# Optimization experiments

Hardware: AMD Instinct MI355X
Metric: run time of the kernel (lower is better)

## Reference

```python
import jax, jax.numpy as jnp
import numpy as np
import math

B, S, D, H = 2, 2048, 1024, 16
DK = D // H


def setup_inputs() -> dict:
    key = jax.random.key(0)
    ks = jax.random.split(key, 10)
    sc = 1.0 / math.sqrt(D)
    inp = {
        "Q_input": jax.random.normal(ks[0], (B, S, D), dtype=jnp.float32),
        "Wq_w": jax.random.normal(ks[1], (D, D), dtype=jnp.float32) * sc,
        "Wq_b": jnp.zeros((D,), dtype=jnp.float32),
        "Wk_w": jax.random.normal(ks[2], (D, D), dtype=jnp.float32) * sc,
        "Wk_b": jnp.zeros((D,), dtype=jnp.float32),
        "Wv_w": jax.random.normal(ks[3], (D, D), dtype=jnp.float32) * sc,
        "Wv_b": jnp.zeros((D,), dtype=jnp.float32),
        "Wo_w": jax.random.normal(ks[4], (D, D), dtype=jnp.float32) * sc,
        "Wo_b": jnp.zeros((D,), dtype=jnp.float32),
        # causal mask, broadcast over batch and heads: [1,1,S,S]
        "mask": jnp.tril(jnp.ones((S, S), dtype=jnp.int32))[None, None],
    }
    return inp


def reference(Q_input, Wq_w, Wq_b, Wk_w, Wk_b, Wv_w, Wv_b, Wo_w, Wo_b, mask):
    b, s, _ = Q_input.shape
    # linear projections (torch Linear: x @ W^T + b)
    Q = Q_input @ Wq_w.T + Wq_b
    K = Q_input @ Wk_w.T + Wk_b
    V = Q_input @ Wv_w.T + Wv_b
    # [b, h, s, dk]
    Q = Q.reshape(b, s, H, DK).transpose(0, 2, 1, 3)
    K = K.reshape(b, s, H, DK).transpose(0, 2, 1, 3)
    V = V.reshape(b, s, H, DK).transpose(0, 2, 1, 3)
    scores = jnp.einsum("bhqd,bhkd->bhqk", Q, K) / math.sqrt(DK)
    scores = jnp.where(mask == 0, jnp.float32(-1e9), scores)
    weights = jax.nn.softmax(scores, axis=-1)
    attn = jnp.einsum("bhqk,bhkd->bhqd", weights, V)
    attn = attn.transpose(0, 2, 1, 3).reshape(b, s, D)
    return attn @ Wo_w.T + Wo_b
```

## Files before the change

### kernel.cpp

```cpp
#include <hip/hip_runtime.h>
#include <hip/hip_bf16.h>
#include <cstdint>

typedef __attribute__((ext_vector_type(8))) short short8;
typedef __attribute__((ext_vector_type(4))) float f32x4;
typedef __attribute__((ext_vector_type(2))) unsigned int uint2v;
typedef unsigned short ushort_t;

#define S_LEN 2048
#define D_DIM 1024
#define NH 16
#define DK 64
#define BATCH 2
#define M_ROWS (BATCH * S_LEN)
#define BK 32

__device__ inline ushort_t f2bf(float f) {
    union { float f; uint32_t u; } v; v.f = f;
    uint32_t r = v.u + 0x7fffu + ((v.u >> 16) & 1u);
    return (ushort_t)(r >> 16);
}

__device__ __forceinline__ ushort_t bfc(float f) {
    __hip_bfloat16 h = __float2bfloat16(f);
    return __builtin_bit_cast(ushort_t, h);
}

__device__ __forceinline__ void glds16(const ushort_t* g, ushort_t* l) {
    __builtin_amdgcn_global_load_lds(
        (const __attribute__((address_space(1))) uint32_t*)g,
        (__attribute__((address_space(3))) uint32_t*)l,
        16, 0, 0);
}

__device__ __forceinline__ float red_max4(float x) {
#if __has_builtin(__builtin_amdgcn_permlane16_swap) && __has_builtin(__builtin_amdgcn_permlane32_swap)
    uint2v a = __builtin_amdgcn_permlane16_swap(__float_as_uint(x), __float_as_uint(x), false, false);
    float y = fmaxf(__uint_as_float(a.x), __uint_as_float(a.y));
    uint2v b = __builtin_amdgcn_permlane32_swap(__float_as_uint(y), __float_as_uint(y), false, false);
    return fmaxf(__uint_as_float(b.x), __uint_as_float(b.y));
#else
    x = fmaxf(x, __shfl_xor(x, 16));
    return fmaxf(x, __shfl_xor(x, 32));
#endif
}
__device__ __forceinline__ float red_sum4(float x) {
#if __has_builtin(__builtin_amdgcn_permlane16_swap) && __has_builtin(__builtin_amdgcn_permlane32_swap)
    uint2v a = __builtin_amdgcn_permlane16_swap(__float_as_uint(x), __float_as_uint(x), false, false);
    float y = __uint_as_float(a.x) + __uint_as_float(a.y);
    uint2v b = __builtin_amdgcn_permlane32_swap(__float_as_uint(y), __float_as_uint(y), false, false);
    return __uint_as_float(b.x) + __uint_as_float(b.y);
#else
    x += __shfl_xor(x, 16);
    return x + __shfl_xor(x, 32);
#endif
}

__global__ void cvt_bf16(const float* __restrict__ in, ushort_t* __restrict__ out, int n4) {
    int i = blockIdx.x * blockDim.x + threadIdx.x;
    int stride = gridDim.x * blockDim.x;
    for (int idx = i; idx < n4; idx += stride) {
        float4 v = ((const float4*)in)[idx];
        ushort4 o;
        o.x = f2bf(v.x); o.y = f2bf(v.y); o.z = f2bf(v.z); o.w = f2bf(v.w);
        ((ushort4*)out)[idx] = o;
    }
}

__global__ void cvt_w3(const float* __restrict__ wq, const float* __restrict__ wk,
                       const float* __restrict__ wv, ushort_t* __restrict__ wqkv) {
    const int seg = (D_DIM * D_DIM) / 4;
    int i = blockIdx.x * blockDim.x + threadIdx.x;
    int stride = gridDim.x * blockDim.x;
    for (int idx = i; idx < 3 * seg; idx += stride) {
        int sel = idx >> 18;
        int id = idx & (seg - 1);
        const float* src = sel == 0 ? wq : (sel == 1 ? wk : wv);
        float4 v = ((const float4*)src)[id];
        ushort4 o;
        o.x = f2bf(v.x); o.y = f2bf(v.y); o.z = f2bf(v.z); o.w = f2bf(v.w);
        ((ushort4*)wqkv)[sel * seg + id] = o;
    }
}

template<int MODE, int BMt, int BNt>
__global__ __launch_bounds__(256) void gemm_bt(const ushort_t* __restrict__ A,
                                               const ushort_t* __restrict__ Bw,
                                               const float* __restrict__ b0,
                                               const float* __restrict__ b1,
                                               const float* __restrict__ b2,
                                               void* __restrict__ C0,
                                               void* __restrict__ C1,
                                               void* __restrict__ C2,
                                               int M, int N, int K) {
    constexpr int FM = BMt / 32, FN = BNt / 32;
    constexpr int ACH = BMt / 64, BCH = BNt / 64;
    __shared__ ushort_t As[BMt * BK];
    __shared__ ushort_t Bs[BNt * BK];
    int tid = threadIdx.x;
    int lane = tid & 63;
    int w = tid >> 6;
    int wr = w >> 1, wc = w & 1;
    int ntile = N / BNt;
    int m0 = (blockIdx.x / ntile) * BMt;
    int n0 = (blockIdx.x % ntile) * BNt;
    int lr = lane & 15;
    int lk = (lane >> 4) * 8;
    int srow = lane >> 2;
    int scol = (lane & 3) * 8;

    f32x4 acc[FM][FN] = {};

    for (int kt = 0; kt < K; kt += BK) {
        __syncthreads();
#pragma unroll
        for (int c = 0; c < ACH; c++)
            glds16(&A[(size_t)(m0 + w * (BMt / 4) + c * 16 + srow) * K + kt + scol],
                   &As[(w * (BMt / 4) + c * 16) * BK]);
#pragma unroll
        for (int c = 0; c < BCH; c++)
            glds16(&Bw[(size_t)(n0 + w * (BNt / 4) + c * 16 + srow) * K + kt + scol],
                   &Bs[(w * (BNt / 4) + c * 16) * BK]);
        __syncthreads();

        short8 af[FM], bf[FN];
#pragma unroll
        for (int f = 0; f < FM; f++)
            af[f] = *(const short8*)&As[(wr * (BMt / 2) + f * 16 + lr) * BK + lk];
#pragma unroll
        for (int f = 0; f < FN; f++)
            bf[f] = *(const short8*)&Bs[(wc * (BNt / 2) + f * 16 + lr) * BK + lk];
#pragma unroll
        for (int i = 0; i < FM; i++)
#pragma unroll
            for (int j = 0; j < FN; j++)
                acc[i][j] = __builtin_amdgcn_mfma_f32_16x16x32_bf16(af[i], bf[j], acc[i][j], 0, 0, 0);
    }

    int r0 = (lane >> 4) * 4;
#pragma unroll
    for (int j = 0; j < FN; j++) {
        int ncol = n0 + wc * (BNt / 2) + j * 16 + lr;
        if (MODE == 2) {
            float bv = b0[ncol];
#pragma unroll
            for (int i = 0; i < FM; i++) {
                int mbase = m0 + wr * (BMt / 2) + i * 16 + r0;
#pragma unroll
                for (int r = 0; r < 4; r++)
                    ((float*)C0)[(size_t)(mbase + r) * N + ncol] = acc[i][j][r] + bv;
            }
        } else {
            int sel = n0 >> 10;
            const float* bp = sel == 0 ? b0 : (sel == 1 ? b1 : b2);
            int nc = ncol & 1023;
            float bv = bp[nc];
            int hh = nc >> 6, dk = nc & 63;
            ushort_t* Co = (ushort_t*)(sel == 0 ? C0 : (sel == 1 ? C1 : C2));
#pragma unroll
            for (int i = 0; i < FM; i++) {
                int mbase = m0 + wr * (BMt / 2) + i * 16 + r0;
                int bb = mbase >> 11, ss = mbase & 2047;
                if (sel == 2) {
                    ushort4 pk;
                    pk.x = f2bf(acc[i][j][0] + bv);
                    pk.y = f2bf(acc[i][j][1] + bv);
                    pk.z = f2bf(acc[i][j][2] + bv);
                    pk.w = f2bf(acc[i][j][3] + bv);
                    size_t idx = ((size_t)(bb * NH + hh) * DK + dk) * S_LEN + ss;
                    *(ushort4*)&Co[idx] = pk;
                } else {
#pragma unroll
                    for (int r = 0; r < 4; r++) {
                        size_t idx = ((size_t)(bb * NH + hh) * S_LEN + (ss + r)) * DK + dk;
                        Co[idx] = f2bf(acc[i][j][r] + bv);
                    }
                }
            }
        }
    }
}

#define CSC 0.1803368801f

__global__ __launch_bounds__(256) void attn_fwd(const ushort_t* __restrict__ Q,
                                                const ushort_t* __restrict__ K,
                                                const ushort_t* __restrict__ Vt,
                                                ushort_t* __restrict__ Oa) {
    __shared__ ushort_t Ks[2][64 * 64];
    __shared__ ushort_t Vs[2][64 * 64];
    __shared__ ushort_t Ps[4][32][72];

    int tid = threadIdx.x;
    int lane = tid & 63;
    int w = tid >> 6;
    int bh = blockIdx.x;
    int jb = blockIdx.y;
    size_t base = (size_t)bh * S_LEN * DK;

    int lr = lane & 15;
    int lk = (lane >> 4) * 8;
    int g16 = (lane >> 4) * 16;
    int r0 = (lane >> 4) * 4;

    auto swz = [](int row, int cb) { return (row * 128 + (cb ^ ((row & 7) << 4))) >> 1; };

    int qbase[2];
    qbase[0] = jb * 64 + w * 16;
    qbase[1] = (31 - jb) * 64 + w * 16;
    int NT = 32 - jb;

    short8 qf[2][2];
#pragma unroll
    for (int qi = 0; qi < 2; qi++) {
        int qrow = qbase[qi] + lr;
        qf[qi][0] = *(const short8*)&Q[base + (size_t)qrow * DK + lk];
        qf[qi][1] = *(const short8*)&Q[base + (size_t)qrow * DK + 32 + lk];
    }

    f32x4 o[4][2] = {};
    float mrowL[2] = {-1e30f, -1e30f};
    float lrow[2] = {0.f, 0.f};

    int sr = tid >> 3;
    int scb = (tid & 7) * 16;
    int sce = (tid & 7) * 8;

    *(uint4*)&Ks[0][swz(sr, scb)]      = *(const uint4*)&K [base + (size_t)sr * DK + sce];
    *(uint4*)&Ks[0][swz(sr + 32, scb)] = *(const uint4*)&K [base + (size_t)(sr + 32) * DK + sce];
    *(uint4*)&Vs[0][swz(sr, scb)]      = *(const uint4*)&Vt[base + (size_t)sr * S_LEN + sce];
    *(uint4*)&Vs[0][swz(sr + 32, scb)] = *(const uint4*)&Vt[base + (size_t)(sr + 32) * S_LEN + sce];
    __syncthreads();

    int cur = 0;
    for (int t = 0; t < NT; ++t) {
        int kv0 = t * 64;
        bool last = (t == NT - 1);
        uint4 kr0, kr1, vr0, vr1;
        if (!last) {
            int tn = t + 1;
            kr0 = *(const uint4*)&K [base + (size_t)(tn * 64 + sr) * DK + sce];
            kr1 = *(const uint4*)&K [base + (size_t)(tn * 64 + sr + 32) * DK + sce];
            vr0 = *(const uint4*)&Vt[base + (size_t)sr * S_LEN + tn * 64 + sce];
            vr1 = *(const uint4*)&Vt[base + (size_t)(sr + 32) * S_LEN + tn * 64 + sce];
        }
        bool act0 = (t <= jb);

        f32x4 st[2][4] = {};
        __builtin_amdgcn_s_setprio(1);
#pragma unroll
        for (int n = 0; n < 4; n++) {
            short8 kf0 = *(const short8*)&Ks[cur][swz(n * 16 + lr, g16)];
            short8 kf1 = *(const short8*)&Ks[cur][swz(n * 16 + lr, 64 + g16)];
            st[1][n] = __builtin_amdgcn_mfma_f32_16x16x32_bf16(kf0, qf[1][0], st[1][n], 0, 0, 0);
            st[1][n] = __builtin_amdgcn_mfma_f32_16x16x32_bf16(kf1, qf[1][1], st[1][n], 0, 0, 0);
            if (act0) {
                st[0][n] = __builtin_amdgcn_mfma_f32_16x16x32_bf16(kf0, qf[0][0], st[0][n], 0, 0, 0);
                st[0][n] = __builtin_amdgcn_mfma_f32_16x16x32_bf16(kf1, qf[0][1], st[0][n], 0, 0, 0);
            }
        }
        __builtin_amdgcn_s_setprio(0);

#pragma unroll
        for (int qi = 0; qi < 2; qi++) {
            if (qi == 0 && !act0) continue;
            int qcol = qbase[qi] + lr;
            if (kv0 + 63 > qbase[qi]) {
#pragma unroll
                for (int n = 0; n < 4; n++)
#pragma unroll
                    for (int i = 0; i < 4; i++) {
                        int kvg = kv0 + n * 16 + r0 + i;
                        if (kvg > qcol) st[qi][n][i] = -1e30f;
                    }
            }
            float mx = fmaxf(
                fmaxf(fmaxf(fmaxf(st[qi][0][0], st[qi][0][1]), fmaxf(st[qi][0][2], st[qi][0][3])),
                      fmaxf(fmaxf(st[qi][1][0], st[qi][1][1]), fmaxf(st[qi][1][2], st[qi][1][3]))),
                fmaxf(fmaxf(fmaxf(st[qi][2][0], st[qi][2][1]), fmaxf(st[qi][2][2], st[qi][2][3])),
                      fmaxf(fmaxf(st[qi][3][0], st[qi][3][1]), fmaxf(st[qi][3][2], st[qi][3][3]))));
            float mxL = red_max4(mx) * CSC;

            bool skip = __all(mxL <= mrowL[qi] + 8.0f);
            float corr = 1.0f;
            float mnewL = mrowL[qi];
            if (!skip) {
                mnewL = fmaxf(mrowL[qi], mxL);
                corr = exp2f(mrowL[qi] - mnewL);
                mrowL[qi] = mnewL;
            }

            float psum = 0.f;
#pragma unroll
            for (int n = 0; n < 4; n++) {
                ushort4 pk;
#pragma unroll
                for (int i = 0; i < 4; i++) {
                    float p = exp2f(fmaf(st[qi][n][i], CSC, -mnewL));
                    st[qi][n][i] = p;
                    psum += p;
                }
                pk.x = bfc(st[qi][n][0]);
                pk.y = bfc(st[qi][n][1]);
                pk.z = bfc(st[qi][n][2]);
                pk.w = bfc(st[qi][n][3]);
                *(ushort4*)&Ps[w][qi * 16 + lr][n * 16 + r0] = pk;
            }
            psum = red_sum4(psum);

            if (skip) {
                lrow[qi] += psum;
            } else {
                lrow[qi] = lrow[qi] * corr + psum;
                float cb[4];
#pragma unroll
                for (int i = 0; i < 4; i++) cb[i] = __shfl(corr, r0 + i);
#pragma unroll
                for (int d = 0; d < 4; d++)
#pragma unroll
                    for (int i = 0; i < 4; i++) o[d][qi][i] *= cb[i];
            }
        }

        short8 pf1[2], pf0[2];
#pragma unroll
        for (int ks = 0; ks < 2; ks++)
            pf1[ks] = *(const short8*)&Ps[w][16 + lr][ks * 32 + lk];
        if (act0)
#pragma unroll
            for (int ks = 0; ks < 2; ks++)
                pf0[ks] = *(const short8*)&Ps[w][lr][ks * 32 + lk];
        __builtin_amdgcn_s_setprio(1);
#pragma unroll
        for (int d = 0; d < 4; d++)
#pragma unroll
            for (int ks = 0; ks < 2; ks++) {
                short8 vf = *(const short8*)&Vs[cur][swz(d * 16 + lr, ks * 64 + g16)];
                o[d][1] = __builtin_amdgcn_mfma_f32_16x16x32_bf16(pf1[ks], vf, o[d][1], 0, 0, 0);
                if (act0)
                    o[d][0] = __builtin_amdgcn_mfma_f32_16x16x32_bf16(pf0[ks], vf, o[d][0], 0, 0, 0);
            }
        __builtin_amdgcn_s_setprio(0);

        if (!last) {
            *(uint4*)&Ks[cur ^ 1][swz(sr, scb)]      = kr0;
            *(uint4*)&Ks[cur ^ 1][swz(sr + 32, scb)] = kr1;
            *(uint4*)&Vs[cur ^ 1][swz(sr, scb)]      = vr0;
            *(uint4*)&Vs[cur ^ 1][swz(sr + 32, scb)] = vr1;
        }
        __syncthreads();
        cur ^= 1;
    }

    int b = bh >> 4, h = bh & 15;
#pragma unroll
    for (int qi = 0; qi < 2; qi++) {
        float lb[4];
#pragma unroll
        for (int i = 0; i < 4; i++) lb[i] = __shfl(lrow[qi], r0 + i);
#pragma unroll
        for (int d = 0; d < 4; d++)
#pragma unroll
            for (int i = 0; i < 4; i++) {
                int qq = qbase[qi] + r0 + i;
                int dk = d * 16 + lr;
                size_t idx = ((size_t)(b * S_LEN + qq)) * D_DIM + h * DK + dk;
                Oa[idx] = bfc(o[d][qi][i] / lb[i]);
            }
    }
}

extern "C" void kernel_launch(void* const* d_in, const int* in_sizes, int n_in,
                              void* d_out, int out_size, void* d_ws, size_t ws_size,
                              hipStream_t stream) {
    const float* X  = (const float*)d_in[0];
    const float* Wq = (const float*)d_in[1];
    const float* bq = (const float*)d_in[2];
    const float* Wk = (const float*)d_in[3];
    const float* bk = (const float*)d_in[4];
    const float* Wv = (const float*)d_in[5];
    const float* bv = (const float*)d_in[6];
    const float* Wo = (const float*)d_in[7];
    const float* bo = (const float*)d_in[8];
    float* out = (float*)d_out;

    char* ws = (char*)d_ws;
    ushort_t* Xb    = (ushort_t*)ws;
    ushort_t* Wqkvb = (ushort_t*)(ws + (8u  << 20));
    ushort_t* Qb    = (ushort_t*)(ws + (14u << 20));
    ushort_t* Kb    = (ushort_t*)(ws + (22u << 20));
    ushort_t* Vtb   = (ushort_t*)(ws + (30u << 20));
    ushort_t* Wob   = Wqkvb;
    ushort_t* Ab    = Xb;

    const int M = M_ROWS;
    int nX4 = (M * D_DIM) / 4;
    int nW4 = (D_DIM * D_DIM) / 4;

    cvt_bf16<<<2048, 256, 0, stream>>>(X, Xb, nX4);
    cvt_w3<<<2048, 256, 0, stream>>>(Wq, Wk, Wv, Wqkvb);

    gemm_bt<3, 128, 128><<<dim3((M / 128) * (3072 / 128)), 256, 0, stream>>>(
        Xb, Wqkvb, bq, bk, bv, Qb, Kb, Vtb, M, 3072, D_DIM);

    cvt_bf16<<<2048, 256, 0, stream>>>(Wo, Wob, nW4);

    dim3 agrid(BATCH * NH, 16);
    attn_fwd<<<agrid, 256, 0, stream>>>(Qb, Kb, Vtb, Ab);

    gemm_bt<2, 64, 128><<<dim3((M / 64) * (D_DIM / 128)), 256, 0, stream>>>(
        Ab, Wob, bo, bo, bo, out, out, out, M, D_DIM, D_DIM);
}
```

Before: 138.0 us.

## Split attention into one query tile per block and route P via permlane

The attention kernel no longer pairs two query tiles (early and late) per block. Each block now handles one 64-row query tile, giving twice as many blocks, with an interleaved tile order to balance the causal work. The P matrix is passed from the QK accumulator layout to the PV operand layout with permlane swaps in registers, so the shared-memory round trip is gone. MFMAs for fully masked sub-tiles on the diagonal are skipped. In exchange, K/V tiles are reloaded for each query tile instead of being shared by two.

New measurement: 135.0 us. 1.02x faster.

```diff
diff --git a/kernel.cpp b/kernel.cpp
--- a/kernel.cpp
+++ b/kernel.cpp
@@ -33,8 +33,14 @@
         16, 0, 0);
 }
 
+#if __has_builtin(__builtin_amdgcn_permlane16_swap) && __has_builtin(__builtin_amdgcn_permlane32_swap)
+#define HAS_PLSWAP 1
+#else
+#define HAS_PLSWAP 0
+#endif
+
 __device__ __forceinline__ float red_max4(float x) {
-#if __has_builtin(__builtin_amdgcn_permlane16_swap) && __has_builtin(__builtin_amdgcn_permlane32_swap)
+#if HAS_PLSWAP
     uint2v a = __builtin_amdgcn_permlane16_swap(__float_as_uint(x), __float_as_uint(x), false, false);
     float y = fmaxf(__uint_as_float(a.x), __uint_as_float(a.y));
     uint2v b = __builtin_amdgcn_permlane32_swap(__float_as_uint(y), __float_as_uint(y), false, false);
@@ -45,7 +51,7 @@
 #endif
 }
 __device__ __forceinline__ float red_sum4(float x) {
-#if __has_builtin(__builtin_amdgcn_permlane16_swap) && __has_builtin(__builtin_amdgcn_permlane32_swap)
+#if HAS_PLSWAP
     uint2v a = __builtin_amdgcn_permlane16_swap(__float_as_uint(x), __float_as_uint(x), false, false);
     float y = __uint_as_float(a.x) + __uint_as_float(a.y);
     uint2v b = __builtin_amdgcn_permlane32_swap(__float_as_uint(y), __float_as_uint(y), false, false);
@@ -53,6 +59,36 @@
 #else
     x += __shfl_xor(x, 16);
     return x + __shfl_xor(x, 32);
+#endif
+}
+
+__device__ __forceinline__ void route_p(const uint32_t wp[4][2], int ks, int lane, uint32_t F[4]) {
+#if HAS_PLSWAP
+    uint32_t U0 = wp[2 * ks][0],     U1 = wp[2 * ks][1];
+    uint32_t V0 = wp[2 * ks + 1][0], V1 = wp[2 * ks + 1][1];
+    uint2v t, pa0, pa1, pb0, pb1;
+    t = __builtin_amdgcn_permlane32_swap(U0, U0, false, false);
+    pa0 = __builtin_amdgcn_permlane16_swap(U0, t.y, false, false);
+    t = __builtin_amdgcn_permlane32_swap(U1, U1, false, false);
+    pa1 = __builtin_amdgcn_permlane16_swap(U1, t.y, false, false);
+    t = __builtin_amdgcn_permlane32_swap(V0, V0, false, false);
+    pb0 = __builtin_amdgcn_permlane16_swap(t.x, V0, false, false);
+    t = __builtin_amdgcn_permlane32_swap(V1, V1, false, false);
+    pb1 = __builtin_amdgcn_permlane16_swap(t.x, V1, false, false);
+    bool lo = lane < 32;
+    F[0] = lo ? pa0.x : pb0.x;
+    F[1] = lo ? pa1.x : pb1.x;
+    F[2] = lo ? pa0.y : pb0.y;
+    F[3] = lo ? pa1.y : pb1.y;
+#else
+    int q = lane & 15, g = lane >> 4;
+#pragma unroll
+    for (int m = 0; m < 4; m++) {
+        int src = 16 * (2 * (g & 1) + (m >> 1)) + q;
+        uint32_t xa = (uint32_t)__shfl((int)wp[2 * ks][m & 1], src);
+        uint32_t xb = (uint32_t)__shfl((int)wp[2 * ks + 1][m & 1], src);
+        F[m] = (g < 2) ? xa : xb;
+    }
 #endif
 }
 
@@ -189,42 +225,36 @@
                                                 ushort_t* __restrict__ Oa) {
     __shared__ ushort_t Ks[2][64 * 64];
     __shared__ ushort_t Vs[2][64 * 64];
-    __shared__ ushort_t Ps[4][32][72];
 
     int tid = threadIdx.x;
     int lane = tid & 63;
     int w = tid >> 6;
     int bh = blockIdx.x;
-    int jb = blockIdx.y;
+    int yy = blockIdx.y;
+    int a = yy >> 3, bsel = yy & 7;
+    int qt = (a == 0) ? bsel : (a == 1) ? 15 - bsel : (a == 2) ? 16 + bsel : 31 - bsel;
     size_t base = (size_t)bh * S_LEN * DK;
+    int q0 = qt * 64;
 
     int lr = lane & 15;
     int lk = (lane >> 4) * 8;
     int g16 = (lane >> 4) * 16;
     int r0 = (lane >> 4) * 4;
+    int wq = w * 16 + lr;
 
     auto swz = [](int row, int cb) { return (row * 128 + (cb ^ ((row & 7) << 4))) >> 1; };
 
-    int qbase[2];
-    qbase[0] = jb * 64 + w * 16;
-    qbase[1] = (31 - jb) * 64 + w * 16;
-    int NT = 32 - jb;
-
-    short8 qf[2][2];
-#pragma unroll
-    for (int qi = 0; qi < 2; qi++) {
-        int qrow = qbase[qi] + lr;
-        qf[qi][0] = *(const short8*)&Q[base + (size_t)qrow * DK + lk];
-        qf[qi][1] = *(const short8*)&Q[base + (size_t)qrow * DK + 32 + lk];
-    }
-
-    f32x4 o[4][2] = {};
-    float mrowL[2] = {-1e30f, -1e30f};
-    float lrow[2] = {0.f, 0.f};
+    short8 qf0 = *(const short8*)&Q[base + (size_t)(q0 + wq) * DK + lk];
+    short8 qf1 = *(const short8*)&Q[base + (size_t)(q0 + wq) * DK + 32 + lk];
+
+    f32x4 o[4] = {};
+    float mrowL = -1e30f, lrow = 0.f;
 
     int sr = tid >> 3;
     int scb = (tid & 7) * 16;
     int sce = (tid & 7) * 8;
+
+    int NT = qt + 1;
 
     *(uint4*)&Ks[0][swz(sr, scb)]      = *(const uint4*)&K [base + (size_t)sr * DK + sce];
     *(uint4*)&Ks[0][swz(sr + 32, scb)] = *(const uint4*)&K [base + (size_t)(sr + 32) * DK + sce];
@@ -234,8 +264,8 @@
 
     int cur = 0;
     for (int t = 0; t < NT; ++t) {
-        int kv0 = t * 64;
         bool last = (t == NT - 1);
+        bool diag = (t == qt);
         uint4 kr0, kr1, vr0, vr1;
         if (!last) {
             int tn = t + 1;
@@ -244,103 +274,88 @@
             vr0 = *(const uint4*)&Vt[base + (size_t)sr * S_LEN + tn * 64 + sce];
             vr1 = *(const uint4*)&Vt[base + (size_t)(sr + 32) * S_LEN + tn * 64 + sce];
         }
-        bool act0 = (t <= jb);
-
-        f32x4 st[2][4] = {};
+
+        f32x4 st[4] = {};
         __builtin_amdgcn_s_setprio(1);
 #pragma unroll
         for (int n = 0; n < 4; n++) {
-            short8 kf0 = *(const short8*)&Ks[cur][swz(n * 16 + lr, g16)];
-            short8 kf1 = *(const short8*)&Ks[cur][swz(n * 16 + lr, 64 + g16)];
-            st[1][n] = __builtin_amdgcn_mfma_f32_16x16x32_bf16(kf0, qf[1][0], st[1][n], 0, 0, 0);
-            st[1][n] = __builtin_amdgcn_mfma_f32_16x16x32_bf16(kf1, qf[1][1], st[1][n], 0, 0, 0);
-            if (act0) {
-                st[0][n] = __builtin_amdgcn_mfma_f32_16x16x32_bf16(kf0, qf[0][0], st[0][n], 0, 0, 0);
-                st[0][n] = __builtin_amdgcn_mfma_f32_16x16x32_bf16(kf1, qf[0][1], st[0][n], 0, 0, 0);
+            if (!diag || n <= w) {
+                short8 kf0 = *(const short8*)&Ks[cur][swz(n * 16 + lr, g16)];
+                short8 kf1 = *(const short8*)&Ks[cur][swz(n * 16 + lr, 64 + g16)];
+                st[n] = __builtin_amdgcn_mfma_f32_16x16x32_bf16(kf0, qf0, st[n], 0, 0, 0);
+                st[n] = __builtin_amdgcn_mfma_f32_16x16x32_bf16(kf1, qf1, st[n], 0, 0, 0);
             }
         }
         __builtin_amdgcn_s_setprio(0);
 
-#pragma unroll
-        for (int qi = 0; qi < 2; qi++) {
-            if (qi == 0 && !act0) continue;
-            int qcol = qbase[qi] + lr;
-            if (kv0 + 63 > qbase[qi]) {
-#pragma unroll
-                for (int n = 0; n < 4; n++)
-#pragma unroll
-                    for (int i = 0; i < 4; i++) {
-                        int kvg = kv0 + n * 16 + r0 + i;
-                        if (kvg > qcol) st[qi][n][i] = -1e30f;
-                    }
+        if (diag) {
+#pragma unroll
+            for (int n = 0; n < 4; n++)
+#pragma unroll
+                for (int i = 0; i < 4; i++)
+                    if (16 * n + r0 + i > wq) st[n][i] = -1e30f;
+        }
+
+        float mx = fmaxf(
+            fmaxf(fmaxf(fmaxf(st[0][0], st[0][1]), fmaxf(st[0][2], st[0][3])),
+                  fmaxf(fmaxf(st[1][0], st[1][1]), fmaxf(st[1][2], st[1][3]))),
+            fmaxf(fmaxf(fmaxf(st[2][0], st[2][1]), fmaxf(st[2][2], st[2][3])),
+                  fmaxf(fmaxf(st[3][0], st[3][1]), fmaxf(st[3][2], st[3][3]))));
+        float mxL = red_max4(mx) * CSC;
+
+        bool skip = __all(mxL <= mrowL + 8.0f);
+        float corr = 1.0f;
+        float mnewL = mrowL;
+        if (!skip) {
+            mnewL = fmaxf(mrowL, mxL);
+            corr = exp2f(mrowL - mnewL);
+            mrowL = mnewL;
+        }
+
+        float psum = 0.f;
+        uint32_t wp[4][2];
+#pragma unroll
+        for (int n = 0; n < 4; n++) {
+#pragma unroll
+            for (int i = 0; i < 4; i++) {
+                float p = exp2f(fmaf(st[n][i], CSC, -mnewL));
+                st[n][i] = p;
+                psum += p;
             }
-            float mx = fmaxf(
-                fmaxf(fmaxf(fmaxf(st[qi][0][0], st[qi][0][1]), fmaxf(st[qi][0][2], st[qi][0][3])),
-                      fmaxf(fmaxf(st[qi][1][0], st[qi][1][1]), fmaxf(st[qi][1][2], st[qi][1][3]))),
-                fmaxf(fmaxf(fmaxf(st[qi][2][0], st[qi][2][1]), fmaxf(st[qi][2][2], st[qi][2][3])),
-                      fmaxf(fmaxf(st[qi][3][0], st[qi][3][1]), fmaxf(st[qi][3][2], st[qi][3][3]))));
-            float mxL = red_max4(mx) * CSC;
-
-            bool skip = __all(mxL <= mrowL[qi] + 8.0f);
-            float corr = 1.0f;
-            float mnewL = mrowL[qi];
-            if (!skip) {
-                mnewL = fmaxf(mrowL[qi], mxL);
-                corr = exp2f(mrowL[qi] - mnewL);
-                mrowL[qi] = mnewL;
+            wp[n][0] = (uint32_t)bfc(st[n][0]) | ((uint32_t)bfc(st[n][1]) << 16);
+            wp[n][1] = (uint32_t)bfc(st[n][2]) | ((uint32_t)bfc(st[n][3]) << 16);
+        }
+        psum = red_sum4(psum);
+
+        if (skip) {
+            lrow += psum;
+        } else {
+            lrow = lrow * corr + psum;
+            float cb[4];
+#pragma unroll
+            for (int i = 0; i < 4; i++) cb[i] = __shfl(corr, r0 + i);
+#pragma unroll
+            for (int d = 0; d < 4; d++)
+#pragma unroll
+                for (int i = 0; i < 4; i++) o[d][i] *= cb[i];
+        }
+
+#pragma unroll
+        for (int ks = 0; ks < 2; ks++) {
+            if (diag && 32 * ks > w * 16 + 15) continue;
+            uint32_t F[4];
+            route_p(wp, ks, lane, F);
+            union { uint32_t u[4]; short8 s; } pu;
+            pu.u[0] = F[0]; pu.u[1] = F[1]; pu.u[2] = F[2]; pu.u[3] = F[3];
+            short8 pf = pu.s;
+            __builtin_amdgcn_s_setprio(1);
+#pragma unroll
+            for (int d = 0; d < 4; d++) {
+                short8 vf = *(const short8*)&Vs[cur][swz(d * 16 + lr, ks * 64 + g16)];
+                o[d] = __builtin_amdgcn_mfma_f32_16x16x32_bf16(pf, vf, o[d], 0, 0, 0);
             }
-
-            float psum = 0.f;
-#pragma unroll
-            for (int n = 0; n < 4; n++) {
-                ushort4 pk;
-#pragma unroll
-                for (int i = 0; i < 4; i++) {
-                    float p = exp2f(fmaf(st[qi][n][i], CSC, -mnewL));
-                    st[qi][n][i] = p;
-                    psum += p;
-                }
-                pk.x = bfc(st[qi][n][0]);
-                pk.y = bfc(st[qi][n][1]);
-                pk.z = bfc(st[qi][n][2]);
-                pk.w = bfc(st[qi][n][3]);
-                *(ushort4*)&Ps[w][qi * 16 + lr][n * 16 + r0] = pk;
-            }
-            psum = red_sum4(psum);
-
-            if (skip) {
-                lrow[qi] += psum;
-            } else {
-                lrow[qi] = lrow[qi] * corr + psum;
-                float cb[4];
-#pragma unroll
-                for (int i = 0; i < 4; i++) cb[i] = __shfl(corr, r0 + i);
-#pragma unroll
-                for (int d = 0; d < 4; d++)
-#pragma unroll
-                    for (int i = 0; i < 4; i++) o[d][qi][i] *= cb[i];
-            }
-        }
-
-        short8 pf1[2], pf0[2];
-#pragma unroll
-        for (int ks = 0; ks < 2; ks++)
-            pf1[ks] = *(const short8*)&Ps[w][16 + lr][ks * 32 + lk];
-        if (act0)
-#pragma unroll
-            for (int ks = 0; ks < 2; ks++)
-                pf0[ks] = *(const short8*)&Ps[w][lr][ks * 32 + lk];
-        __builtin_amdgcn_s_setprio(1);
-#pragma unroll
-        for (int d = 0; d < 4; d++)
-#pragma unroll
-            for (int ks = 0; ks < 2; ks++) {
-                short8 vf = *(const short8*)&Vs[cur][swz(d * 16 + lr, ks * 64 + g16)];
-                o[d][1] = __builtin_amdgcn_mfma_f32_16x16x32_bf16(pf1[ks], vf, o[d][1], 0, 0, 0);
-                if (act0)
-                    o[d][0] = __builtin_amdgcn_mfma_f32_16x16x32_bf16(pf0[ks], vf, o[d][0], 0, 0, 0);
-            }
-        __builtin_amdgcn_s_setprio(0);
+            __builtin_amdgcn_s_setprio(0);
+        }
 
         if (!last) {
             *(uint4*)&Ks[cur ^ 1][swz(sr, scb)]      = kr0;
@@ -353,21 +368,18 @@
     }
 
     int b = bh >> 4, h = bh & 15;
-#pragma unroll
-    for (int qi = 0; qi < 2; qi++) {
-        float lb[4];
-#pragma unroll
-        for (int i = 0; i < 4; i++) lb[i] = __shfl(lrow[qi], r0 + i);
-#pragma unroll
-        for (int d = 0; d < 4; d++)
-#pragma unroll
-            for (int i = 0; i < 4; i++) {
-                int qq = qbase[qi] + r0 + i;
-                int dk = d * 16 + lr;
-                size_t idx = ((size_t)(b * S_LEN + qq)) * D_DIM + h * DK + dk;
-                Oa[idx] = bfc(o[d][qi][i] / lb[i]);
-            }
-    }
+    float lb[4];
+#pragma unroll
+    for (int i = 0; i < 4; i++) lb[i] = __shfl(lrow, r0 + i);
+#pragma unroll
+    for (int d = 0; d < 4; d++)
+#pragma unroll
+        for (int i = 0; i < 4; i++) {
+            int qq = q0 + w * 16 + r0 + i;
+            int dk = d * 16 + lr;
+            size_t idx = ((size_t)(b * S_LEN + qq)) * D_DIM + h * DK + dk;
+            Oa[idx] = bfc(o[d][i] / lb[i]);
+        }
 }
 
 extern "C" void kernel_launch(void* const* d_in, const int* in_sizes, int n_in,
@@ -405,7 +417,7 @@
 
     cvt_bf16<<<2048, 256, 0, stream>>>(Wo, Wob, nW4);
 
-    dim3 agrid(BATCH * NH, 16);
+    dim3 agrid(BATCH * NH, 32);
     attn_fwd<<<agrid, 256, 0, stream>>>(Qb, Kb, Vtb, Ab);
 
     gemm_bt<2, 64, 128><<<dim3((M / 64) * (D_DIM / 128)), 256, 0, stream>>>(
```
